# Performance work log

Measured on AMD Instinct MI355X. Metric: run time of the kernel, lower is better.

Reference implementation:

```python
import jax, jax.numpy as jnp
import numpy as np

N, C, K, M = 100000, 128, 27, 4  # voxels, channels, 3^3 kernel offsets, branches
EPS = 1e-5


def setup_inputs() -> dict:
    key = jax.random.key(0)
    ks = jax.random.split(key, 4)
    x = jax.random.normal(ks[0], (N, C), jnp.float32)
    # neighbor index per voxel per kernel offset (Minkowski kernel map)
    nbr_idx = jax.random.randint(ks[1], (N, K), 0, N, dtype=jnp.int32)
    W1 = jax.random.normal(ks[2], (M, C, C), jnp.float32) * (1.0 / np.sqrt(C))
    g1 = jnp.ones((M, C), jnp.float32)
    b1 = jnp.zeros((M, C), jnp.float32)
    wk = jax.random.normal(ks[3], (M, K, C), jnp.float32) * (1.0 / np.sqrt(K))
    g_out = jnp.ones((C,), jnp.float32)
    b_out = jnp.zeros((C,), jnp.float32)
    return {"x": x, "nbr_idx": nbr_idx, "W1": W1, "g1": g1, "b1": b1,
            "wk": wk, "g_out": g_out, "b_out": b_out}


def _bn(h, g, b):
    # training-mode batch norm over the voxel axis
    mu = h.mean(0)
    var = h.var(0)
    return (h - mu) * jax.lax.rsqrt(var + EPS) * g + b


def reference(x, nbr_idx, W1, g1, b1, wk, g_out, b_out):
    out = jnp.zeros_like(x)
    for m in range(M):  # fixed small branch count
        # Conv1x1 (pointwise) + BN + ReLU
        h = jax.nn.relu(_bn(x @ W1[m], g1[m], b1[m]))  # [N, C]
        # channelwise 3^3 sparse conv: gather neighbor, per-channel scale, accumulate
        acc = jnp.zeros_like(h)
        for k in range(K):  # fixed 27 kernel offsets; avoids [N,K,C] materialization
            acc = acc + h[nbr_idx[:, k]] * wk[m, k]
        out = out + acc  # stack(-1).sum(-1) over branches
    out = jax.nn.relu(_bn(out, g_out, b_out))  # out_bn_relu
    out = out + x  # residual (inplanes == planes)
    return jax.nn.relu(out)  # final nonlinearity ('ReLU')
```

## Files before the change

### kernel.cpp

```cpp
#include <hip/hip_runtime.h>

#define KK 27
#define EPSV 1e-5f

typedef __attribute__((ext_vector_type(8))) short bf16x8;
typedef __attribute__((ext_vector_type(4))) float f32x4;
typedef __attribute__((ext_vector_type(4))) unsigned int u32x4;

static __device__ __forceinline__ unsigned short f2bf(float f) {
    unsigned u = __float_as_uint(f);
    u = u + 0x7fffu + ((u >> 16) & 1u);
    return (unsigned short)(u >> 16);
}

static __device__ __forceinline__ unsigned short f2h(float f) {
    _Float16 h = (_Float16)f;
    unsigned short u;
    __builtin_memcpy(&u, &h, 2);
    return u;
}
static __device__ __forceinline__ float h2f(unsigned short s) {
    _Float16 h;
    __builtin_memcpy(&h, &s, 2);
    return (float)h;
}
static __device__ __forceinline__ float hlo(unsigned u) { return h2f((unsigned short)(u & 0xffffu)); }
static __device__ __forceinline__ float hhi(unsigned u) { return h2f((unsigned short)(u >> 16)); }

__global__ void k0_wt(const float* __restrict__ W1, unsigned short* __restrict__ WT) {
    int m = blockIdx.x >> 7, n = blockIdx.x & 127, k = threadIdx.x;
    WT[((m * 128 + n) * 128) + k] = f2bf(W1[(m * 128 + k) * 128 + n]);
}

__launch_bounds__(256)
__global__ void kA_gemm(const float* __restrict__ x, const unsigned short* __restrict__ WT,
                        unsigned short* __restrict__ Yall, float* __restrict__ ysum_b,
                        float* __restrict__ ysq_b, int binstride, int binmask,
                        int N, int m0, int m1, int ystride) {
    __shared__ unsigned short As[64 * 136];
    __shared__ unsigned short Bs[128 * 136];
    const int t = threadIdx.x;
    const int i0 = blockIdx.x * 64;
    const int binoff = (blockIdx.x & binmask) * binstride;

#pragma unroll
    for (int it = 0; it < 8; ++it) {
        int flat = it * 256 + t;
        int r = flat >> 5, c4 = (flat & 31) * 4;
        float4 v = make_float4(0.f, 0.f, 0.f, 0.f);
        if (i0 + r < N) v = *(const float4*)(x + (size_t)(i0 + r) * 128 + c4);
        ushort4 bb;
        bb.x = f2bf(v.x); bb.y = f2bf(v.y); bb.z = f2bf(v.z); bb.w = f2bf(v.w);
        *(ushort4*)(As + r * 136 + c4) = bb;
    }

    const int w = t >> 6, lane = t & 63;
    const int wr = w >> 1, wc = w & 1;
    const int r16 = lane & 15, q = lane >> 4;

    for (int m = m0; m < m1; ++m) {
        __syncthreads();
        const uint4* Wp = (const uint4*)(WT + (size_t)m * 128 * 128);
#pragma unroll
        for (int it = 0; it < 8; ++it) {
            int flat = it * 256 + t;
            int n = flat >> 4, kc = flat & 15;
            uint4 v = Wp[n * 16 + kc];
            *(uint4*)(Bs + n * 136 + kc * 8) = v;
        }
        __syncthreads();

        f32x4 acc[2][4];
#pragma unroll
        for (int a = 0; a < 2; ++a)
#pragma unroll
            for (int b = 0; b < 4; ++b) { acc[a][b][0] = 0.f; acc[a][b][1] = 0.f; acc[a][b][2] = 0.f; acc[a][b][3] = 0.f; }

#pragma unroll
        for (int ks = 0; ks < 4; ++ks) {
            int ko = ks * 32 + q * 8;
            bf16x8 af[2], bfr[4];
#pragma unroll
            for (int ri = 0; ri < 2; ++ri)
                af[ri] = *(const bf16x8*)(As + (wr * 32 + ri * 16 + r16) * 136 + ko);
#pragma unroll
            for (int ci = 0; ci < 4; ++ci)
                bfr[ci] = *(const bf16x8*)(Bs + (wc * 64 + ci * 16 + r16) * 136 + ko);
#pragma unroll
            for (int ri = 0; ri < 2; ++ri)
#pragma unroll
                for (int ci = 0; ci < 4; ++ci)
                    acc[ri][ci] = __builtin_amdgcn_mfma_f32_16x16x32_bf16(af[ri], bfr[ci], acc[ri][ci], 0, 0, 0);
        }

#pragma unroll
        for (int ci = 0; ci < 4; ++ci) {
            float s = 0.f, s2 = 0.f;
#pragma unroll
            for (int ri = 0; ri < 2; ++ri) {
#pragma unroll
                for (int r = 0; r < 4; ++r) {
                    int row = i0 + wr * 32 + ri * 16 + q * 4 + r;
                    float vv = acc[ri][ci][r];
                    if (row < N) { s += vv; s2 += vv * vv; }
                }
            }
            s  += __shfl_xor(s, 16);  s  += __shfl_xor(s, 32);
            s2 += __shfl_xor(s2, 16); s2 += __shfl_xor(s2, 32);
            if (lane < 16) {
                int col = wc * 64 + ci * 16 + r16;
                atomicAdd(ysum_b + binoff + m * 128 + col, s);
                atomicAdd(ysq_b  + binoff + m * 128 + col, s2);
            }
        }

        __syncthreads();
        unsigned short* Ys = Bs;
#pragma unroll
        for (int ci = 0; ci < 4; ++ci) {
            int col = wc * 64 + ci * 16 + r16;
#pragma unroll
            for (int ri = 0; ri < 2; ++ri) {
#pragma unroll
                for (int r = 0; r < 4; ++r) {
                    int rl = wr * 32 + ri * 16 + q * 4 + r;
                    Ys[rl * 136 + col] = f2h(acc[ri][ci][r]);
                }
            }
        }
        __syncthreads();
        const int cb = (m - m0) * 128;
#pragma unroll
        for (int it = 0; it < 4; ++it) {
            int chunk = it * 256 + t;
            int row = chunk >> 4, c8 = (chunk & 15) * 8;
            if (i0 + row < N) {
                u32x4 v = *(const u32x4*)(Ys + row * 136 + c8);
                __builtin_nontemporal_store(v, (u32x4*)(Yall + (size_t)(i0 + row) * ystride + cb + c8));
            }
        }
    }
}

__global__ void k2_coef(const float* __restrict__ ysum_b, const float* __restrict__ ysq_b,
                        int nbin, int binstride,
                        const float* __restrict__ g1, const float* __restrict__ b1,
                        float* __restrict__ a1, float* __restrict__ c1, int N, int m0) {
    int tid = blockIdx.x * blockDim.x + threadIdx.x;
    int c = tid & 127;
    int m = m0 + (tid >> 7);
    int idx = (tid);
    float s = 0.f, s2 = 0.f;
    for (int b = 0; b < nbin; ++b) {
        s  += ysum_b[b * binstride + idx];
        s2 += ysq_b [b * binstride + idx];
    }
    float mean = s / (float)N;
    float var  = s2 / (float)N - mean * mean;
    float a = g1[m * 128 + c] * rsqrtf(var + EPSV);
    a1[m * 128 + c] = a;
    c1[m * 128 + c] = b1[m * 128 + c] - mean * a;
}

__launch_bounds__(256)
__global__ void k4_all(const unsigned short* __restrict__ Y, const int* __restrict__ nbr,
                       const float* __restrict__ wkg, const float* __restrict__ A1g,
                       const float* __restrict__ C1g, float* __restrict__ P,
                       float* __restrict__ osum_b, float* __restrict__ osq_b, int N) {
    __shared__ unsigned short wkL[4 * KK * 136];
    __shared__ float ssum[128], ssq[128];
    const int t = threadIdx.x;
    for (int idx = t; idx < 4 * KK * 128; idx += 256) {
        int c = idx & 127, km = idx >> 7;
        wkL[km * 136 + c] = f2h(wkg[idx]);
    }
    if (t < 128) { ssum[t] = 0.f; ssq[t] = 0.f; }

    const int lane = t & 63;
    const int m = lane >> 4, c16 = lane & 15;
    const int q = m;
    const unsigned short* wbase = wkL + (m * KK) * 136 + c16 * 8;
    const unsigned short* hbase = Y + lane * 8;

    float Ar[8], Cr[8];
    {
        const float4 A0 = *(const float4*)(A1g + m * 128 + c16 * 8);
        const float4 A1 = *(const float4*)(A1g + m * 128 + c16 * 8 + 4);
        const float4 C0 = *(const float4*)(C1g + m * 128 + c16 * 8);
        const float4 C1 = *(const float4*)(C1g + m * 128 + c16 * 8 + 4);
        Ar[0]=A0.x; Ar[1]=A0.y; Ar[2]=A0.z; Ar[3]=A0.w;
        Ar[4]=A1.x; Ar[5]=A1.y; Ar[6]=A1.z; Ar[7]=A1.w;
        Cr[0]=C0.x; Cr[1]=C0.y; Cr[2]=C0.z; Cr[3]=C0.w;
        Cr[4]=C1.x; Cr[5]=C1.y; Cr[6]=C1.z; Cr[7]=C1.w;
    }
    __syncthreads();

    float os[8], oq[8];
#pragma unroll
    for (int e = 0; e < 8; ++e) { os[e] = 0.f; oq[e] = 0.f; }

    const int wid = blockIdx.x * 4 + (t >> 6);
    const int nw  = gridDim.x * 4;
    const int ng  = (N + 3) >> 2;
    for (int vg = wid; vg < ng; vg += nw) {
        const int v0 = __builtin_amdgcn_readfirstlane(vg << 2);
        const int* np = nbr + (size_t)v0 * KK;
        const int o1 = (v0 + 1 < N) ? KK : 0;
        const int o2 = (v0 + 2 < N) ? 2 * KK : 0;
        const int o3 = (v0 + 3 < N) ? 3 * KK : 0;
        float acc0[8], acc1[8], acc2[8], acc3[8];
#pragma unroll
        for (int e = 0; e < 8; ++e) { acc0[e] = 0.f; acc1[e] = 0.f; acc2[e] = 0.f; acc3[e] = 0.f; }

#pragma unroll 3
        for (int k = 0; k < KK; ++k) {
            const int j0 = np[k];
            const int j1 = np[o1 + k];
            const int j2 = np[o2 + k];
            const int j3 = np[o3 + k];
            const uint4 hv0 = *(const uint4*)(hbase + ((size_t)j0 << 9));
            const uint4 hv1 = *(const uint4*)(hbase + ((size_t)j1 << 9));
            const uint4 hv2 = *(const uint4*)(hbase + ((size_t)j2 << 9));
            const uint4 hv3 = *(const uint4*)(hbase + ((size_t)j3 << 9));
            const uint4 wv  = *(const uint4*)(wbase + k * 136);
            const float w0 = hlo(wv.x), w1 = hhi(wv.x), w2 = hlo(wv.y), w3 = hhi(wv.y);
            const float w4 = hlo(wv.z), w5 = hhi(wv.z), w6 = hlo(wv.w), w7 = hhi(wv.w);
#define K4BODY(A, H)                                                        \
            A[0] += fmaxf(0.f, hlo(H.x) * Ar[0] + Cr[0]) * w0;              \
            A[1] += fmaxf(0.f, hhi(H.x) * Ar[1] + Cr[1]) * w1;              \
            A[2] += fmaxf(0.f, hlo(H.y) * Ar[2] + Cr[2]) * w2;              \
            A[3] += fmaxf(0.f, hhi(H.y) * Ar[3] + Cr[3]) * w3;              \
            A[4] += fmaxf(0.f, hlo(H.z) * Ar[4] + Cr[4]) * w4;              \
            A[5] += fmaxf(0.f, hhi(H.z) * Ar[5] + Cr[5]) * w5;              \
            A[6] += fmaxf(0.f, hlo(H.w) * Ar[6] + Cr[6]) * w6;              \
            A[7] += fmaxf(0.f, hhi(H.w) * Ar[7] + Cr[7]) * w7;
            K4BODY(acc0, hv0)
            K4BODY(acc1, hv1)
            K4BODY(acc2, hv2)
            K4BODY(acc3, hv3)
#undef K4BODY
        }

#pragma unroll
        for (int e = 0; e < 8; ++e) {
            acc0[e] += __shfl_xor(acc0[e], 16); acc0[e] += __shfl_xor(acc0[e], 32);
            acc1[e] += __shfl_xor(acc1[e], 16); acc1[e] += __shfl_xor(acc1[e], 32);
            acc2[e] += __shfl_xor(acc2[e], 16); acc2[e] += __shfl_xor(acc2[e], 32);
            acc3[e] += __shfl_xor(acc3[e], 16); acc3[e] += __shfl_xor(acc3[e], 32);
        }
        float av[8];
#pragma unroll
        for (int e = 0; e < 8; ++e)
            av[e] = (q == 0) ? acc0[e] : (q == 1) ? acc1[e] : (q == 2) ? acc2[e] : acc3[e];
        const int vq = v0 + q;
        if (vq < N) {
            f32x4 x0 = {av[0], av[1], av[2], av[3]};
            f32x4 x1 = {av[4], av[5], av[6], av[7]};
            float* p = P + (size_t)vq * 128 + c16 * 8;
            __builtin_nontemporal_store(x0, (f32x4*)p);
            __builtin_nontemporal_store(x1, (f32x4*)(p + 4));
#pragma unroll
            for (int e = 0; e < 8; ++e) { os[e] += av[e]; oq[e] += av[e] * av[e]; }
        }
    }

#pragma unroll
    for (int e = 0; e < 8; ++e) {
        atomicAdd(ssum + c16 * 8 + e, os[e]);
        atomicAdd(ssq  + c16 * 8 + e, oq[e]);
    }
    __syncthreads();
    if (t < 128) {
        const int bo = (blockIdx.x & 3) * 128;
        atomicAdd(osum_b + bo + t, ssum[t]);
        atomicAdd(osq_b  + bo + t, ssq[t]);
    }
}

template <int MODE>
__launch_bounds__(256)
__global__ void k4_gather(const unsigned short* __restrict__ Ym, int ystride,
                          const int* __restrict__ nbr,
                          const float* __restrict__ wkm, const float* __restrict__ a1m,
                          const float* __restrict__ c1m, float* __restrict__ P,
                          float* __restrict__ osum, float* __restrict__ osq, int N) {
    __shared__ float wkL[KK * 132];
    __shared__ float ssum[128], ssq[128];
    const int t = threadIdx.x;
    for (int idx = t; idx < KK * 128; idx += 256) {
        int k = idx >> 7, c = idx & 127;
        wkL[k * 132 + c] = wkm[k * 128 + c];
    }
    if (MODE == 2) { if (t < 128) { ssum[t] = 0.f; ssq[t] = 0.f; } }

    const int w = t >> 6, lane = t & 63;
    const int q = lane >> 4, c16 = lane & 15;
    const int slot = w * 4 + q;
    const int vox = blockIdx.x * 16 + slot;
    const bool alive = vox < N;

    float aR[8], cR[8];
    {
        const float4 A0 = *(const float4*)(a1m + c16 * 8);
        const float4 A1 = *(const float4*)(a1m + c16 * 8 + 4);
        const float4 C0 = *(const float4*)(c1m + c16 * 8);
        const float4 C1 = *(const float4*)(c1m + c16 * 8 + 4);
        aR[0]=A0.x; aR[1]=A0.y; aR[2]=A0.z; aR[3]=A0.w;
        aR[4]=A1.x; aR[5]=A1.y; aR[6]=A1.z; aR[7]=A1.w;
        cR[0]=C0.x; cR[1]=C0.y; cR[2]=C0.z; cR[3]=C0.w;
        cR[4]=C1.x; cR[5]=C1.y; cR[6]=C1.z; cR[7]=C1.w;
    }
    __syncthreads();

    const long long base = alive ? (long long)vox * KK : 0;
    float acc[8];
#pragma unroll
    for (int e = 0; e < 8; ++e) acc[e] = 0.f;

#pragma unroll 3
    for (int k = 0; k < KK; ++k) {
        int j = nbr[base + k];
        const uint4 hv = *(const uint4*)(Ym + (size_t)j * ystride + c16 * 8);
        const float4 wa = *(const float4*)(wkL + k * 132 + c16 * 8);
        const float4 wb = *(const float4*)(wkL + k * 132 + c16 * 8 + 4);
        float h0 = fmaxf(0.f, hlo(hv.x) * aR[0] + cR[0]);
        float h1 = fmaxf(0.f, hhi(hv.x) * aR[1] + cR[1]);
        float h2 = fmaxf(0.f, hlo(hv.y) * aR[2] + cR[2]);
        float h3 = fmaxf(0.f, hhi(hv.y) * aR[3] + cR[3]);
        float h4 = fmaxf(0.f, hlo(hv.z) * aR[4] + cR[4]);
        float h5 = fmaxf(0.f, hhi(hv.z) * aR[5] + cR[5]);
        float h6 = fmaxf(0.f, hlo(hv.w) * aR[6] + cR[6]);
        float h7 = fmaxf(0.f, hhi(hv.w) * aR[7] + cR[7]);
        acc[0] += h0 * wa.x; acc[1] += h1 * wa.y;
        acc[2] += h2 * wa.z; acc[3] += h3 * wa.w;
        acc[4] += h4 * wb.x; acc[5] += h5 * wb.y;
        acc[6] += h6 * wb.z; acc[7] += h7 * wb.w;
    }

    float os[8], oq[8];
    if (alive) {
        float* p = P + (size_t)vox * 128 + c16 * 8;
        if (MODE == 0) {
            float4 v0 = {acc[0], acc[1], acc[2], acc[3]};
            float4 v1 = {acc[4], acc[5], acc[6], acc[7]};
            *(float4*)p = v0;
            *(float4*)(p + 4) = v1;
        } else {
            float4 o0 = *(const float4*)p, o1 = *(const float4*)(p + 4);
            o0.x += acc[0]; o0.y += acc[1]; o0.z += acc[2]; o0.w += acc[3];
            o1.x += acc[4]; o1.y += acc[5]; o1.z += acc[6]; o1.w += acc[7];
            *(float4*)p = o0;
            *(float4*)(p + 4) = o1;
            if (MODE == 2) {
                os[0] = o0.x; oq[0] = o0.x * o0.x;
                os[1] = o0.y; oq[1] = o0.y * o0.y;
                os[2] = o0.z; oq[2] = o0.z * o0.z;
                os[3] = o0.w; oq[3] = o0.w * o0.w;
                os[4] = o1.x; oq[4] = o1.x * o1.x;
                os[5] = o1.y; oq[5] = o1.y * o1.y;
                os[6] = o1.z; oq[6] = o1.z * o1.z;
                os[7] = o1.w; oq[7] = o1.w * o1.w;
            }
        }
    }
    if (MODE == 2) {
        if (!alive) {
#pragma unroll
            for (int e = 0; e < 8; ++e) { os[e] = 0.f; oq[e] = 0.f; }
        }
#pragma unroll
        for (int e = 0; e < 8; ++e) {
            os[e] += __shfl_xor(os[e], 16); os[e] += __shfl_xor(os[e], 32);
            oq[e] += __shfl_xor(oq[e], 16); oq[e] += __shfl_xor(oq[e], 32);
        }
        if (lane < 16) {
#pragma unroll
            for (int e = 0; e < 8; ++e) {
                atomicAdd(ssum + c16 * 8 + e, os[e]);
                atomicAdd(ssq  + c16 * 8 + e, oq[e]);
            }
        }
        __syncthreads();
        if (t < 128) {
            atomicAdd(osum + t, ssum[t]);
            atomicAdd(osq  + t, ssq[t]);
        }
    }
}

__global__ void k5_coef(const float* __restrict__ osum_b, const float* __restrict__ osq_b,
                        int nbin,
                        const float* __restrict__ g, const float* __restrict__ b,
                        float* __restrict__ ao, float* __restrict__ co, int N) {
    int c = threadIdx.x;
    float s = 0.f, s2 = 0.f;
    for (int bi = 0; bi < nbin; ++bi) {
        s  += osum_b[bi * 128 + c];
        s2 += osq_b [bi * 128 + c];
    }
    float mean = s / (float)N;
    float var  = s2 / (float)N - mean * mean;
    float a = g[c] * rsqrtf(var + EPSV);
    ao[c] = a;
    co[c] = b[c] - mean * a;
}

__launch_bounds__(256)
__global__ void k6_final(float* __restrict__ P, const float* __restrict__ x,
                         const float* __restrict__ ao, const float* __restrict__ co, int N) {
    long long t4 = ((long long)blockIdx.x * 256 + threadIdx.x) * 4;
    if (t4 >= (long long)N * 128) return;
    int c4 = (int)(t4 & 127);
    float4 p  = *(const float4*)(P + t4);
    float4 xv = *(const float4*)(x + t4);
    float4 a  = *(const float4*)(ao + c4);
    float4 c  = *(const float4*)(co + c4);
    float4 o;
    o.x = fmaxf(0.f, fmaxf(0.f, p.x * a.x + c.x) + xv.x);
    o.y = fmaxf(0.f, fmaxf(0.f, p.y * a.y + c.y) + xv.y);
    o.z = fmaxf(0.f, fmaxf(0.f, p.z * a.z + c.z) + xv.z);
    o.w = fmaxf(0.f, fmaxf(0.f, p.w * a.w + c.w) + xv.w);
    *(float4*)(P + t4) = o;
}

extern "C" void kernel_launch(void* const* d_in, const int* in_sizes, int n_in,
                              void* d_out, int out_size, void* d_ws, size_t ws_size,
                              hipStream_t stream) {
    const float* x     = (const float*)d_in[0];
    const int*   nbr   = (const int*)d_in[1];
    const float* W1    = (const float*)d_in[2];
    const float* g1    = (const float*)d_in[3];
    const float* b1    = (const float*)d_in[4];
    const float* wk    = (const float*)d_in[5];
    const float* g_out = (const float*)d_in[6];
    const float* b_out = (const float*)d_in[7];
    const int N = in_sizes[0] / 128;

    float* P = (float*)d_out;
    char* ws = (char*)d_ws;
    float* ysum = (float*)ws;
    float* ysq  = ysum + 512;
    float* osum = ysq + 512;
    float* osq  = osum + 128;
    float* osb  = osq + 128;
    float* oqb  = osb + 512;
    float* a1   = oqb + 512;
    float* c1   = a1 + 512;
    float* ao   = c1 + 512;
    float* co   = ao + 128;
    unsigned short* WT = (unsigned short*)(ws + 16384);
    unsigned short* Y  = (unsigned short*)(ws + 16384 + 131072);

    const bool fused = ws_size >= (size_t)16384 + 131072 + (size_t)N * 512 * 2;

    hipMemsetAsync(d_ws, 0, 16384, stream);
    k0_wt<<<512, 128, 0, stream>>>(W1, WT);

    const int gA = (N + 63) / 64;
    const int g4 = (N + 15) / 16;

    if (fused) {
        float* ysum_b = P;
        float* ysq_b  = P + 64 * 512;
        hipMemsetAsync(d_out, 0, 64 * 512 * 2 * sizeof(float), stream);
        kA_gemm<<<gA, 256, 0, stream>>>(x, WT, Y, ysum_b, ysq_b, 512, 63, N, 0, 4, 512);
        k2_coef<<<2, 256, 0, stream>>>(ysum_b, ysq_b, 64, 512, g1, b1, a1, c1, N, 0);
        k4_all<<<1280, 256, 0, stream>>>(Y, nbr, wk, a1, c1, P, osb, oqb, N);
        k5_coef<<<1, 128, 0, stream>>>(osb, oqb, 4, g_out, b_out, ao, co, N);
    } else {
        for (int m = 0; m < 4; ++m) {
            kA_gemm<<<gA, 256, 0, stream>>>(x, WT, Y, ysum, ysq, 0, 0, N, m, m + 1, 128);
            k2_coef<<<1, 128, 0, stream>>>(ysum, ysq, 1, 0, g1, b1, a1, c1, N, m);
            if (m == 0)
                k4_gather<0><<<g4, 256, 0, stream>>>(Y, 128, nbr, wk + m * KK * 128,
                                                     a1 + m * 128, c1 + m * 128, P, osum, osq, N);
            else if (m == 3)
                k4_gather<2><<<g4, 256, 0, stream>>>(Y, 128, nbr, wk + m * KK * 128,
                                                     a1 + m * 128, c1 + m * 128, P, osum, osq, N);
            else
                k4_gather<1><<<g4, 256, 0, stream>>>(Y, 128, nbr, wk + m * KK * 128,
                                                     a1 + m * 128, c1 + m * 128, P, osum, osq, N);
        }
        k5_coef<<<1, 128, 0, stream>>>(osum, osq, 1, g_out, b_out, ao, co, N);
    }
    const int g6 = (int)(((long long)N * 128 / 4 + 255) / 256);
    k6_final<<<g6, 256, 0, stream>>>(P, x, ao, co, N);
}
```

Measured before the change: 599.4 us.

## Compute branch BN stats from X^T X Gram matrix instead of per-GEMM atomics

Replaces the per-tile atomic accumulation of the GEMM output sums and squared sums with an algebraic route. A separate kernel forms X^T X and the column sums of x using bf16 MFMA into per-block slabs, which are then reduced. The mean and variance of x@W1[m] are derived as w^T(X^T X)w and colsum·w. The main GEMM runs without the stats epilogue, and the k4_all grid is raised from 1280 to 2048 blocks. This trades the atomics for an extra pass over x plus the slab reduction, and the E[y^2]-mean^2 variance now comes from a bf16-derived Gram matrix, which may lose precision.

```diff
diff --git a/kernel.cpp b/kernel.cpp
--- a/kernel.cpp
+++ b/kernel.cpp
@@ -2,6 +2,7 @@
 
 #define KK 27
 #define EPSV 1e-5f
+#define KS_NB 128
 
 typedef __attribute__((ext_vector_type(8))) short bf16x8;
 typedef __attribute__((ext_vector_type(4))) float f32x4;
@@ -33,15 +34,126 @@
 }
 
 __launch_bounds__(256)
+__global__ void kS_xtx(const float* __restrict__ x, float* __restrict__ slabs,
+                       float* __restrict__ colsum, int N, int nchunk) {
+    __shared__ unsigned short AsT[128 * 68];
+    __shared__ float csL[8 * 128];
+    const int t = threadIdx.x;
+    const int w = t >> 6, lane = t & 63;
+    const int r16 = lane & 15, q = lane >> 4;
+    const int c4 = (t & 31) * 4;
+
+    f32x4 acc[2][8];
+#pragma unroll
+    for (int ri = 0; ri < 2; ++ri)
+#pragma unroll
+        for (int b = 0; b < 8; ++b) { acc[ri][b][0]=0.f; acc[ri][b][1]=0.f; acc[ri][b][2]=0.f; acc[ri][b][3]=0.f; }
+
+    float cs0 = 0.f, cs1 = 0.f, cs2 = 0.f, cs3 = 0.f;
+
+    for (int ch = blockIdx.x; ch < nchunk; ch += KS_NB) {
+        const int i0 = ch * 64;
+        __syncthreads();
+#pragma unroll
+        for (int it = 0; it < 8; ++it) {
+            int r = it * 8 + (t >> 5);
+            float4 v = make_float4(0.f, 0.f, 0.f, 0.f);
+            if (i0 + r < N) v = *(const float4*)(x + (size_t)(i0 + r) * 128 + c4);
+            AsT[(c4 + 0) * 68 + r] = f2bf(v.x);
+            AsT[(c4 + 1) * 68 + r] = f2bf(v.y);
+            AsT[(c4 + 2) * 68 + r] = f2bf(v.z);
+            AsT[(c4 + 3) * 68 + r] = f2bf(v.w);
+            cs0 += v.x; cs1 += v.y; cs2 += v.z; cs3 += v.w;
+        }
+        __syncthreads();
+#pragma unroll
+        for (int kc = 0; kc < 2; ++kc) {
+            bf16x8 f[8];
+#pragma unroll
+            for (int i = 0; i < 8; ++i)
+                f[i] = *(const bf16x8*)(AsT + (i * 16 + r16) * 68 + kc * 32 + q * 8);
+#pragma unroll
+            for (int ri = 0; ri < 2; ++ri)
+#pragma unroll
+                for (int b = 0; b < 8; ++b)
+                    acc[ri][b] = __builtin_amdgcn_mfma_f32_16x16x32_bf16(f[w * 2 + ri], f[b], acc[ri][b], 0, 0, 0);
+        }
+    }
+
+    float* slab = slabs + (size_t)blockIdx.x * 16384;
+#pragma unroll
+    for (int ri = 0; ri < 2; ++ri)
+#pragma unroll
+        for (int b = 0; b < 8; ++b)
+#pragma unroll
+            for (int r = 0; r < 4; ++r) {
+                int row = (w * 2 + ri) * 16 + q * 4 + r;
+                int col = b * 16 + r16;
+                slab[row * 128 + col] = acc[ri][b][r];
+            }
+
+    __syncthreads();
+    csL[(t >> 5) * 128 + c4 + 0] = cs0;
+    csL[(t >> 5) * 128 + c4 + 1] = cs1;
+    csL[(t >> 5) * 128 + c4 + 2] = cs2;
+    csL[(t >> 5) * 128 + c4 + 3] = cs3;
+    __syncthreads();
+    if (t < 128) {
+        float s = 0.f;
+#pragma unroll
+        for (int g = 0; g < 8; ++g) s += csL[g * 128 + t];
+        atomicAdd(colsum + t, s);
+    }
+}
+
+__global__ void kR_reduce(const float* __restrict__ slabs, float* __restrict__ XtX, int nslab) {
+    int t = blockIdx.x * blockDim.x + threadIdx.x;
+    float s = 0.f;
+    for (int sl = 0; sl < nslab; ++sl) s += slabs[(size_t)sl * 16384 + t];
+    XtX[t] = s;
+}
+
+__launch_bounds__(256)
+__global__ void k2b_coef(const float* __restrict__ XtX, const float* __restrict__ colsum,
+                         const float* __restrict__ W1, const float* __restrict__ g1,
+                         const float* __restrict__ b1, float* __restrict__ a1,
+                         float* __restrict__ c1, int N) {
+    const int mc = blockIdx.x, m = mc >> 7, c = mc & 127;
+    __shared__ float wS[128];
+    __shared__ float red[8];
+    const int t = threadIdx.x;
+    if (t < 128) wS[t] = W1[(m * 128 + t) * 128 + c];
+    __syncthreads();
+    const int a = t >> 1, b0 = (t & 1) * 64;
+    float s = 0.f;
+    for (int i = 0; i < 64; ++i) s += XtX[a * 128 + b0 + i] * wS[b0 + i];
+    s *= wS[a];
+    float mp = (t < 128) ? colsum[t] * wS[t] : 0.f;
+#pragma unroll
+    for (int d = 1; d < 64; d <<= 1) { s += __shfl_xor(s, d); mp += __shfl_xor(mp, d); }
+    if ((t & 63) == 0) { red[t >> 6] = s; red[4 + (t >> 6)] = mp; }
+    __syncthreads();
+    if (t == 0) {
+        float sy2 = red[0] + red[1] + red[2] + red[3];
+        float my  = red[4] + red[5] + red[6] + red[7];
+        float mean = my / (float)N;
+        float var  = sy2 / (float)N - mean * mean;
+        float aa = g1[mc] * rsqrtf(var + EPSV);
+        a1[mc] = aa;
+        c1[mc] = b1[mc] - mean * aa;
+    }
+}
+
+template <int STATS>
+__launch_bounds__(256)
 __global__ void kA_gemm(const float* __restrict__ x, const unsigned short* __restrict__ WT,
-                        unsigned short* __restrict__ Yall, float* __restrict__ ysum_b,
-                        float* __restrict__ ysq_b, int binstride, int binmask,
+                        unsigned short* __restrict__ Yall, float* __restrict__ ysum,
+                        float* __restrict__ ysq,
                         int N, int m0, int m1, int ystride) {
     __shared__ unsigned short As[64 * 136];
     __shared__ unsigned short Bs[128 * 136];
     const int t = threadIdx.x;
     const int i0 = blockIdx.x * 64;
-    const int binoff = (blockIdx.x & binmask) * binstride;
 
 #pragma unroll
     for (int it = 0; it < 8; ++it) {
@@ -93,24 +205,26 @@
                     acc[ri][ci] = __builtin_amdgcn_mfma_f32_16x16x32_bf16(af[ri], bfr[ci], acc[ri][ci], 0, 0, 0);
         }
 
-#pragma unroll
-        for (int ci = 0; ci < 4; ++ci) {
-            float s = 0.f, s2 = 0.f;
-#pragma unroll
-            for (int ri = 0; ri < 2; ++ri) {
-#pragma unroll
-                for (int r = 0; r < 4; ++r) {
-                    int row = i0 + wr * 32 + ri * 16 + q * 4 + r;
-                    float vv = acc[ri][ci][r];
-                    if (row < N) { s += vv; s2 += vv * vv; }
+        if (STATS) {
+#pragma unroll
+            for (int ci = 0; ci < 4; ++ci) {
+                float s = 0.f, s2 = 0.f;
+#pragma unroll
+                for (int ri = 0; ri < 2; ++ri) {
+#pragma unroll
+                    for (int r = 0; r < 4; ++r) {
+                        int row = i0 + wr * 32 + ri * 16 + q * 4 + r;
+                        float vv = acc[ri][ci][r];
+                        if (row < N) { s += vv; s2 += vv * vv; }
+                    }
                 }
-            }
-            s  += __shfl_xor(s, 16);  s  += __shfl_xor(s, 32);
-            s2 += __shfl_xor(s2, 16); s2 += __shfl_xor(s2, 32);
-            if (lane < 16) {
-                int col = wc * 64 + ci * 16 + r16;
-                atomicAdd(ysum_b + binoff + m * 128 + col, s);
-                atomicAdd(ysq_b  + binoff + m * 128 + col, s2);
+                s  += __shfl_xor(s, 16);  s  += __shfl_xor(s, 32);
+                s2 += __shfl_xor(s2, 16); s2 += __shfl_xor(s2, 32);
+                if (lane < 16) {
+                    int col = wc * 64 + ci * 16 + r16;
+                    atomicAdd(ysum + m * 128 + col, s);
+                    atomicAdd(ysq  + m * 128 + col, s2);
+                }
             }
         }
 
@@ -142,21 +256,13 @@
     }
 }
 
-__global__ void k2_coef(const float* __restrict__ ysum_b, const float* __restrict__ ysq_b,
-                        int nbin, int binstride,
+__global__ void k2_coef(const float* __restrict__ ysum, const float* __restrict__ ysq,
                         const float* __restrict__ g1, const float* __restrict__ b1,
                         float* __restrict__ a1, float* __restrict__ c1, int N, int m0) {
-    int tid = blockIdx.x * blockDim.x + threadIdx.x;
-    int c = tid & 127;
-    int m = m0 + (tid >> 7);
-    int idx = (tid);
-    float s = 0.f, s2 = 0.f;
-    for (int b = 0; b < nbin; ++b) {
-        s  += ysum_b[b * binstride + idx];
-        s2 += ysq_b [b * binstride + idx];
-    }
-    float mean = s / (float)N;
-    float var  = s2 / (float)N - mean * mean;
+    int c = threadIdx.x & 127;
+    int m = m0 + (threadIdx.x >> 7);
+    float mean = ysum[m * 128 + c] / (float)N;
+    float var  = ysq[m * 128 + c] / (float)N - mean * mean;
     float a = g1[m * 128 + c] * rsqrtf(var + EPSV);
     a1[m * 128 + c] = a;
     c1[m * 128 + c] = b1[m * 128 + c] - mean * a;
@@ -448,6 +554,7 @@
     float* c1   = a1 + 512;
     float* ao   = c1 + 512;
     float* co   = ao + 128;
+    float* colsum = co + 128;
     unsigned short* WT = (unsigned short*)(ws + 16384);
     unsigned short* Y  = (unsigned short*)(ws + 16384 + 131072);
 
@@ -458,19 +565,21 @@
 
     const int gA = (N + 63) / 64;
     const int g4 = (N + 15) / 16;
+    const int nchunk = (N + 63) / 64;
 
     if (fused) {
-        float* ysum_b = P;
-        float* ysq_b  = P + 64 * 512;
-        hipMemsetAsync(d_out, 0, 64 * 512 * 2 * sizeof(float), stream);
-        kA_gemm<<<gA, 256, 0, stream>>>(x, WT, Y, ysum_b, ysq_b, 512, 63, N, 0, 4, 512);
-        k2_coef<<<2, 256, 0, stream>>>(ysum_b, ysq_b, 64, 512, g1, b1, a1, c1, N, 0);
-        k4_all<<<1280, 256, 0, stream>>>(Y, nbr, wk, a1, c1, P, osb, oqb, N);
+        float* slabs = P;
+        float* XtXf  = P + (size_t)KS_NB * 16384;
+        kS_xtx<<<KS_NB, 256, 0, stream>>>(x, slabs, colsum, N, nchunk);
+        kR_reduce<<<64, 256, 0, stream>>>(slabs, XtXf, KS_NB);
+        k2b_coef<<<512, 256, 0, stream>>>(XtXf, colsum, W1, g1, b1, a1, c1, N);
+        kA_gemm<0><<<gA, 256, 0, stream>>>(x, WT, Y, nullptr, nullptr, N, 0, 4, 512);
+        k4_all<<<2048, 256, 0, stream>>>(Y, nbr, wk, a1, c1, P, osb, oqb, N);
         k5_coef<<<1, 128, 0, stream>>>(osb, oqb, 4, g_out, b_out, ao, co, N);
     } else {
         for (int m = 0; m < 4; ++m) {
-            kA_gemm<<<gA, 256, 0, stream>>>(x, WT, Y, ysum, ysq, 0, 0, N, m, m + 1, 128);
-            k2_coef<<<1, 128, 0, stream>>>(ysum, ysq, 1, 0, g1, b1, a1, c1, N, m);
+            kA_gemm<1><<<gA, 256, 0, stream>>>(x, WT, Y, ysum, ysq, N, m, m + 1, 128);
+            k2_coef<<<1, 128, 0, stream>>>(ysum, ysq, g1, b1, a1, c1, N, m);
             if (m == 0)
                 k4_gather<0><<<g4, 256, 0, stream>>>(Y, 128, nbr, wk + m * KK * 128,
                                                      a1 + m * 128, c1 + m * 128, P, osum, osq, N);
```

Result: slower. 933.2 us (+55.7%).
